# Optimization experiments

Measured on AMD Instinct MI355X. Metric: run time of the kernel, lower is better.

The kernel has to match this reference:

```python
import jax, jax.numpy as jnp
import numpy as np

DIM = 512
NUM_HEADS = 8
NUM_BLOCKS = 16
# NOTE: original code computes head_dim from FULL dim (before the reduce layer),
# so scale = (dim // num_heads) ** -0.5 = 64 ** -0.5, even though the actual
# per-head dim after reduce is 32. We preserve this quirk faithfully.
SCALE = (DIM // NUM_HEADS) ** -0.5


def setup_inputs() -> dict:
    key = jax.random.key(0)
    ks = jax.random.split(key, 5)
    B, N = 4, 4096
    C = DIM // 2
    x = jax.random.normal(ks[0], (B, N, DIM), dtype=jnp.float32)
    reduce_w = jax.random.normal(ks[1], (DIM, C), dtype=jnp.float32) * (DIM ** -0.5)
    qkv_w = jax.random.normal(ks[2], (C, 3 * C), dtype=jnp.float32) * (C ** -0.5)
    proj_w = jax.random.normal(ks[3], (C, DIM), dtype=jnp.float32) * (C ** -0.5)
    proj_b = jnp.zeros((DIM,), dtype=jnp.float32)
    return {"x": x, "reduce_w": reduce_w, "qkv_w": qkv_w,
            "proj_w": proj_w, "proj_b": proj_b}


def reference(x, reduce_w, qkv_w, proj_w, proj_b):
    B, N, _ = x.shape
    xr = x @ reduce_w                      # [B, N, C]  (C = dim/2)
    C = xr.shape[-1]
    H = NUM_HEADS
    d = C // H
    qkv = (xr @ qkv_w).reshape(B, N, 3, H, d).transpose(2, 0, 3, 1, 4)  # [3,B,H,N,d]
    q, k, v = qkv[0], qkv[1], qkv[2]
    bs = N // NUM_BLOCKS                   # block (chunk) size
    # block-diagonal local attention: reshape seq into independent blocks
    qb = q.reshape(B, H, NUM_BLOCKS, bs, d)
    kb = k.reshape(B, H, NUM_BLOCKS, bs, d)
    vb = v.reshape(B, H, NUM_BLOCKS, bs, d)
    attn = jnp.einsum('bhnqd,bhnkd->bhnqk', qb, kb) * SCALE
    attn = jax.nn.softmax(attn, axis=-1)
    ob = jnp.einsum('bhnqk,bhnkd->bhnqd', attn, vb)   # [B,H,Nb,bs,d]
    # torch: per-block transpose(1,2) then cat on dim=1 -> [B, N, H, d]
    o = ob.transpose(0, 2, 3, 1, 4).reshape(B, N, C)
    return o @ proj_w + proj_b
```

## Files before the change

### kernel.cpp

```cpp
#include <hip/hip_runtime.h>
#include <hip/hip_fp16.h>

typedef _Float16 half_t;
typedef _Float16 f16x8 __attribute__((ext_vector_type(8)));
typedef __fp16 fp16x2 __attribute__((ext_vector_type(2)));
typedef float f32x4 __attribute__((ext_vector_type(4)));

#define MFMA_F16(a, b, c) __builtin_amdgcn_mfma_f32_16x16x32_f16((a), (b), (c), 0, 0, 0)

static __device__ inline unsigned pkrtz(float a, float b) {
    union { fp16x2 h; unsigned u; } c;
    c.h = __builtin_amdgcn_cvt_pkrtz(a, b);
    return c.u;
}

__global__ __launch_bounds__(256) void prep(
    const float* __restrict__ qw, const float* __restrict__ rw,
    const float* __restrict__ pw, half_t* __restrict__ pw_t,
    half_t* __restrict__ Wt) {
    __shared__ __align__(16) char smem[24576];
    const int bid = blockIdx.x, tid = threadIdx.x;

    if (bid < 48) {
        char* As = smem;
        char* Bs = smem + 8192;
        const int M0 = (bid % 12) * 64, N0 = (bid / 12) * 128;
        const int lane = tid & 63, w = tid >> 6;
        const int l15 = lane & 15, l4 = lane >> 4;
        const int wrow = (w >> 1) * 32, wcol = (w & 1) * 64;
        const int pa = (l15 & 7) << 4;

        f32x4 acc[2][4];
#pragma unroll
        for (int i = 0; i < 2; ++i)
#pragma unroll
            for (int j = 0; j < 4; ++j) acc[i][j] = (f32x4){0.f, 0.f, 0.f, 0.f};

        for (int kc = 0; kc < 4; ++kc) {
            int c0 = kc * 64;
            __syncthreads();
#pragma unroll
            for (int i = 0; i < 2; ++i) {
                int j = tid + i * 256;
                int row = j >> 3, e8 = (j & 7) * 8;
                float s = (M0 + row) < 256 ? 0.18033688f : 1.f;
                f16x8 v;
#pragma unroll
                for (int e = 0; e < 8; ++e)
                    v[e] = (half_t)(qw[(size_t)(c0 + e8 + e) * 768 + M0 + row] * s);
                *(f16x8*)(As + row * 128 + ((e8 * 2) ^ ((row & 7) << 4))) = v;
            }
#pragma unroll
            for (int i = 0; i < 4; ++i) {
                int j = tid + i * 256;
                int row = j >> 3, e8 = (j & 7) * 8;
                const float* p = rw + (size_t)(N0 + row) * 256 + c0 + e8;
                float4 u0 = *(const float4*)p;
                float4 u1 = *(const float4*)(p + 4);
                f16x8 v;
                v[0] = (half_t)u0.x; v[1] = (half_t)u0.y;
                v[2] = (half_t)u0.z; v[3] = (half_t)u0.w;
                v[4] = (half_t)u1.x; v[5] = (half_t)u1.y;
                v[6] = (half_t)u1.z; v[7] = (half_t)u1.w;
                *(f16x8*)(Bs + row * 128 + ((e8 * 2) ^ ((row & 7) << 4))) = v;
            }
            __syncthreads();
#pragma unroll
            for (int ki = 0; ki < 2; ++ki) {
                f16x8 af[2], bf[4];
#pragma unroll
                for (int mi = 0; mi < 2; ++mi) {
                    int row = wrow + mi * 16 + l15;
                    af[mi] = *(const f16x8*)(As + row * 128 + (((ki * 4 + l4) << 4) ^ pa));
                }
#pragma unroll
                for (int nj = 0; nj < 4; ++nj) {
                    int row = wcol + nj * 16 + l15;
                    bf[nj] = *(const f16x8*)(Bs + row * 128 + (((ki * 4 + l4) << 4) ^ pa));
                }
#pragma unroll
                for (int mi = 0; mi < 2; ++mi)
#pragma unroll
                    for (int nj = 0; nj < 4; ++nj)
                        acc[mi][nj] = MFMA_F16(af[mi], bf[nj], acc[mi][nj]);
            }
        }
#pragma unroll
        for (int mi = 0; mi < 2; ++mi)
#pragma unroll
            for (int nj = 0; nj < 4; ++nj)
#pragma unroll
                for (int reg = 0; reg < 4; ++reg) {
                    int grow = M0 + wrow + mi * 16 + l4 * 4 + reg;
                    int gcol = N0 + wcol + nj * 16 + l15;
                    Wt[(size_t)grow * 512 + gcol] = (half_t)acc[mi][nj][reg];
                }
        return;
    }

    half_t* tile = (half_t*)smem;
    int t = bid - 48;
    int R0 = (t >> 3) * 64, C0 = (t & 7) * 64;
#pragma unroll
    for (int e = 0; e < 16; ++e) {
        int idx = tid + e * 256;
        int r = idx >> 6, c = idx & 63;
        tile[r * 72 + c] = (half_t)pw[(size_t)(R0 + r) * 512 + C0 + c];
    }
    __syncthreads();
#pragma unroll
    for (int e = 0; e < 16; ++e) {
        int idx = tid + e * 256;
        int c = idx >> 6, r = idx & 63;
        pw_t[(size_t)(C0 + c) * 256 + R0 + r] = tile[r * 72 + c];
    }
}

template <int EPI, bool AFP32, int NB, int K>
__global__ __launch_bounds__(512) void gemm_f16(
    const void* __restrict__ Aop, const half_t* __restrict__ Bt,
    void* __restrict__ Dst, const float* __restrict__ bias) {
    constexpr int nkt = K >> 6;
    constexpr int NAC = 2;
    constexpr int NBC = NB / 64;
    constexpr int NJ = NB / 64;
    __shared__ __align__(16) char smem[16384 + NB * 128];
    char* As = smem;
    char* Bs = smem + 16384;

    const int tid = threadIdx.x;
    const int lane = tid & 63, w = tid >> 6;
    const int l15 = lane & 15, l4 = lane >> 4;
    const int wrow = (w >> 2) * 64;
    const int wcol = (w & 3) * (NB / 4);
    const int bm0 = blockIdx.x * 128;
    const int bn0 = blockIdx.y * NB;
    const int pa = (l15 & 7) << 4;

    f32x4 acc[4][NJ];
#pragma unroll
    for (int i = 0; i < 4; ++i)
#pragma unroll
        for (int j = 0; j < NJ; ++j) acc[i][j] = (f32x4){0.f, 0.f, 0.f, 0.f};

    f16x8 aReg[NAC], bReg[NBC];

    auto load_tile = [&](int kt) {
#pragma unroll
        for (int i = 0; i < NAC; ++i) {
            int c = tid + i * 512;
            int row = c >> 3, k0 = (c & 7) * 8;
            int gk = kt * 64 + k0;
            if (AFP32) {
                const float* Af = (const float*)Aop + (size_t)(bm0 + row) * K + gk;
                float4 u0 = *(const float4*)Af;
                float4 u1 = *(const float4*)(Af + 4);
                f16x8 v;
                v[0] = (half_t)u0.x; v[1] = (half_t)u0.y;
                v[2] = (half_t)u0.z; v[3] = (half_t)u0.w;
                v[4] = (half_t)u1.x; v[5] = (half_t)u1.y;
                v[6] = (half_t)u1.z; v[7] = (half_t)u1.w;
                aReg[i] = v;
            } else {
                aReg[i] = *(const f16x8*)((const half_t*)Aop + (size_t)(bm0 + row) * K + gk);
            }
        }
#pragma unroll
        for (int i = 0; i < NBC; ++i) {
            int c = tid + i * 512;
            int row = c >> 3, k0 = (c & 7) * 8;
            bReg[i] = *(const f16x8*)(Bt + (size_t)(bn0 + row) * K + kt * 64 + k0);
        }
    };

    load_tile(0);
    for (int kt = 0; kt < nkt; ++kt) {
        __syncthreads();
#pragma unroll
        for (int i = 0; i < NAC; ++i) {
            int c = tid + i * 512;
            int row = c >> 3, k0 = (c & 7) * 8;
            *(f16x8*)(As + row * 128 + ((k0 * 2) ^ ((row & 7) << 4))) = aReg[i];
        }
#pragma unroll
        for (int i = 0; i < NBC; ++i) {
            int c = tid + i * 512;
            int row = c >> 3, k0 = (c & 7) * 8;
            *(f16x8*)(Bs + row * 128 + ((k0 * 2) ^ ((row & 7) << 4))) = bReg[i];
        }
        __syncthreads();
        if (kt + 1 < nkt) load_tile(kt + 1);
#pragma unroll
        for (int ki = 0; ki < 2; ++ki) {
            f16x8 af[4], bf[NJ];
#pragma unroll
            for (int mi = 0; mi < 4; ++mi) {
                int row = wrow + mi * 16 + l15;
                af[mi] = *(const f16x8*)(As + row * 128 + (((ki * 4 + l4) << 4) ^ pa));
            }
#pragma unroll
            for (int nj = 0; nj < NJ; ++nj) {
                int row = wcol + nj * 16 + l15;
                bf[nj] = *(const f16x8*)(Bs + row * 128 + (((ki * 4 + l4) << 4) ^ pa));
            }
#pragma unroll
            for (int mi = 0; mi < 4; ++mi)
#pragma unroll
                for (int nj = 0; nj < NJ; ++nj)
                    acc[mi][nj] = MFMA_F16(af[mi], bf[nj], acc[mi][nj]);
        }
    }

#pragma unroll
    for (int mi = 0; mi < 4; ++mi) {
#pragma unroll
        for (int nj = 0; nj < NJ; ++nj) {
#pragma unroll
            for (int reg = 0; reg < 4; ++reg) {
                int grow = bm0 + wrow + mi * 16 + l4 * 4 + reg;
                int gcol = bn0 + wcol + nj * 16 + l15;
                float val = acc[mi][nj][reg];
                if (EPI == 1) {
                    int t = gcol >> 8, h = (gcol >> 5) & 7, dd = gcol & 31;
                    int b = grow >> 12, n = grow & 4095;
                    int blk = n >> 8, r = n & 255;
                    size_t idx = (size_t)t * 4194304 +
                                 (size_t)((((b << 3) + h) << 4) + blk) * 8192 +
                                 (size_t)r * 32 + dd;
                    ((half_t*)Dst)[idx] = (half_t)val;
                } else {
                    ((float*)Dst)[(size_t)grow * 512 + gcol] = val + bias[gcol];
                }
            }
        }
    }
}

__global__ __launch_bounds__(512, 4) void attn_f16(const half_t* __restrict__ qkv_ws,
                                                   half_t* __restrict__ o_ws) {
    __shared__ __align__(16) half_t VT[32 * 264];

    const int blkid = blockIdx.x;
    const int b = blkid >> 7, h = (blkid >> 4) & 7, blk = blkid & 15;
    const half_t* Q  = qkv_ws + (size_t)blkid * 8192;
    const half_t* Kp = qkv_ws + 4194304 + (size_t)blkid * 8192;
    const half_t* V  = qkv_ws + 8388608 + (size_t)blkid * 8192;

    const int tid = threadIdx.x, lane = tid & 63, w = tid >> 6;
    const int l15 = lane & 15, l4 = lane >> 4;
    const int qb = w * 32;

#pragma unroll
    for (int i = 0; i < 2; ++i) {
        int c = tid + i * 512;
        int key = c >> 2, k8 = (c & 3) * 8;
        f16x8 v = *(const f16x8*)(V + key * 32 + k8);
#pragma unroll
        for (int e = 0; e < 8; ++e) VT[(k8 + e) * 264 + key] = v[e];
    }

    f16x8 aq[2];
    aq[0] = *(const f16x8*)(Q + (qb + l15) * 32 + l4 * 8);
    aq[1] = *(const f16x8*)(Q + (qb + 16 + l15) * 32 + l4 * 8);

    __syncthreads();

    float s_run[2] = {0.f, 0.f};
    f32x4 acc_o[2][2];
#pragma unroll
    for (int qg = 0; qg < 2; ++qg)
#pragma unroll
        for (int fo = 0; fo < 2; ++fo) acc_o[qg][fo] = (f32x4){0.f, 0.f, 0.f, 0.f};
    const f32x4 zero4 = (f32x4){0.f, 0.f, 0.f, 0.f};

    for (int kt = 0; kt < 4; ++kt) {
        f16x8 ka[4];
#pragma unroll
        for (int t = 0; t < 4; ++t)
            ka[t] = *(const f16x8*)(Kp + (kt * 64 + t * 16 + l15) * 32 + l4 * 8);
        f16x8 bv[2][2];
#pragma unroll
        for (int c = 0; c < 2; ++c)
#pragma unroll
            for (int fo = 0; fo < 2; ++fo)
                bv[c][fo] = *(const f16x8*)&VT[(fo * 16 + l15) * 264 + kt * 64 + c * 32 + l4 * 8];

        f32x4 st[2][4];
        __builtin_amdgcn_s_setprio(1);
#pragma unroll
        for (int qg = 0; qg < 2; ++qg)
#pragma unroll
            for (int t = 0; t < 4; ++t) st[qg][t] = MFMA_F16(ka[t], aq[qg], zero4);
        __builtin_amdgcn_s_setprio(0);

#pragma unroll
        for (int qg = 0; qg < 2; ++qg) {
            float p[4][4];
            float ps = 0.f;
#pragma unroll
            for (int t = 0; t < 4; ++t)
#pragma unroll
                for (int r = 0; r < 4; ++r) {
                    float e = exp2f(st[qg][t][r]);
                    p[t][r] = e;
                    ps += e;
                }
            ps += __shfl_xor(ps, 16);
            ps += __shfl_xor(ps, 32);
            s_run[qg] += ps;

#pragma unroll
            for (int c = 0; c < 2; ++c) {
                unsigned pk0[2], pk1[2];
#pragma unroll
                for (int rp = 0; rp < 2; ++rp) {
                    pk0[rp] = pkrtz(p[2 * c][2 * rp], p[2 * c][2 * rp + 1]);
                    pk1[rp] = pkrtz(p[2 * c + 1][2 * rp], p[2 * c + 1][2 * rp + 1]);
                }
                union { unsigned u[4]; f16x8 v; } au;
#pragma unroll
                for (int j = 0; j < 4; ++j) {
                    int src = l15 + ((((l4 & 1) << 1) + (j >> 1)) << 4);
                    unsigned g0 = (unsigned)__shfl((int)pk0[j & 1], src);
                    unsigned g1 = (unsigned)__shfl((int)pk1[j & 1], src);
                    au.u[j] = (l4 < 2) ? g0 : g1;
                }
                __builtin_amdgcn_s_setprio(1);
#pragma unroll
                for (int fo = 0; fo < 2; ++fo)
                    acc_o[qg][fo] = MFMA_F16(au.v, bv[c][fo], acc_o[qg][fo]);
                __builtin_amdgcn_s_setprio(0);
            }
        }
    }

#pragma unroll
    for (int qg = 0; qg < 2; ++qg) {
        float inv = 1.f / s_run[qg];
        float sinv[4];
#pragma unroll
        for (int r = 0; r < 4; ++r) sinv[r] = __shfl(inv, (l4 << 2) | r);
#pragma unroll
        for (int fo = 0; fo < 2; ++fo)
#pragma unroll
            for (int r = 0; r < 4; ++r) {
                int grow = b * 4096 + blk * 256 + qb + qg * 16 + l4 * 4 + r;
                o_ws[(size_t)grow * 256 + h * 32 + fo * 16 + l15] =
                    (half_t)(acc_o[qg][fo][r] * sinv[r]);
            }
    }
}

extern "C" void kernel_launch(void* const* d_in, const int* in_sizes, int n_in,
                              void* d_out, int out_size, void* d_ws, size_t ws_size,
                              hipStream_t stream) {
    const float* x        = (const float*)d_in[0];
    const float* reduce_w = (const float*)d_in[1];
    const float* qkv_w    = (const float*)d_in[2];
    const float* proj_w   = (const float*)d_in[3];
    const float* proj_b   = (const float*)d_in[4];
    char* ws = (char*)d_ws;

    half_t* qkv_ws = (half_t*)ws;
    half_t* o_buf  = (half_t*)(ws + 25165824);
    half_t* pw_t   = (half_t*)(ws + 33554432);
    half_t* Wt     = (half_t*)(ws + 33816576);

    prep<<<80, 256, 0, stream>>>(qkv_w, reduce_w, proj_w, pw_t, Wt);
    gemm_f16<1, true, 192, 512><<<dim3(128, 4), 512, 0, stream>>>(x, Wt, qkv_ws, nullptr);
    attn_f16<<<512, 512, 0, stream>>>(qkv_ws, o_buf);
    gemm_f16<2, false, 256, 256><<<dim3(128, 2), 512, 0, stream>>>(o_buf, pw_t, d_out, proj_b);
}
```

Baseline: 61.71 us.

## Rewrite QKV GEMM with 32x32 MFMA and 256-row tiles

Replaces the templated GEMM with a dedicated QKV kernel that uses 32x32x16 MFMA instructions, a 256x192 block tile with a 4x2 wave layout, and swizzled global-to-LDS chunk mapping. This halves the grid to 256 blocks, so each block reuses the weight tile across more rows and issues fewer MFMA instructions per FLOP. The projection GEMM is specialised into its own non-templated kernel with unchanged logic. The trade-offs are larger LDS and register use per block and fewer blocks to spread across the CUs.

After: 62.96 us. +2.0%, slower.

```diff
diff --git a/kernel.cpp b/kernel.cpp
--- a/kernel.cpp
+++ b/kernel.cpp
@@ -5,8 +5,10 @@
 typedef _Float16 f16x8 __attribute__((ext_vector_type(8)));
 typedef __fp16 fp16x2 __attribute__((ext_vector_type(2)));
 typedef float f32x4 __attribute__((ext_vector_type(4)));
+typedef float f32x16 __attribute__((ext_vector_type(16)));
 
 #define MFMA_F16(a, b, c) __builtin_amdgcn_mfma_f32_16x16x32_f16((a), (b), (c), 0, 0, 0)
+#define MFMA32_F16(a, b, c) __builtin_amdgcn_mfma_f32_32x32x16_f16((a), (b), (c), 0, 0, 0)
 
 static __device__ inline unsigned pkrtz(float a, float b) {
     union { fp16x2 h; unsigned u; } c;
@@ -116,124 +118,195 @@
     }
 }
 
-template <int EPI, bool AFP32, int NB, int K>
-__global__ __launch_bounds__(512) void gemm_f16(
-    const void* __restrict__ Aop, const half_t* __restrict__ Bt,
-    void* __restrict__ Dst, const float* __restrict__ bias) {
-    constexpr int nkt = K >> 6;
-    constexpr int NAC = 2;
-    constexpr int NBC = NB / 64;
-    constexpr int NJ = NB / 64;
-    __shared__ __align__(16) char smem[16384 + NB * 128];
+__global__ __launch_bounds__(512) void gemm_qkv(
+    const float* __restrict__ X, const half_t* __restrict__ Bt,
+    half_t* __restrict__ Dst) {
+    __shared__ __align__(16) char smem[32768 + 24576];
+    char* As = smem;
+    char* Bs = smem + 32768;
+
+    const int tid = threadIdx.x;
+    const int lane = tid & 63, wv = tid >> 6;
+    const int l31 = lane & 31, kh = lane >> 5;
+    const int wrow = (wv >> 1) * 64, wcol = (wv & 1) * 96;
+    const int bm0 = blockIdx.x * 256;
+    const int bn0 = blockIdx.y * 192;
+
+    f32x16 acc[2][3];
+#pragma unroll
+    for (int i = 0; i < 2; ++i)
+#pragma unroll
+        for (int j = 0; j < 3; ++j) acc[i][j] = (f32x16)(0.f);
+
+    f16x8 aReg[4], bReg[3];
+
+    auto load_tile = [&](int kt) {
+#pragma unroll
+        for (int i = 0; i < 4; ++i) {
+            int J = tid + i * 512;
+            int row = J >> 3, c = (J & 7) ^ (row & 7);
+            const float* p = X + (size_t)(bm0 + row) * 512 + kt * 64 + c * 8;
+            float4 u0 = *(const float4*)p;
+            float4 u1 = *(const float4*)(p + 4);
+            f16x8 v;
+            v[0] = (half_t)u0.x; v[1] = (half_t)u0.y;
+            v[2] = (half_t)u0.z; v[3] = (half_t)u0.w;
+            v[4] = (half_t)u1.x; v[5] = (half_t)u1.y;
+            v[6] = (half_t)u1.z; v[7] = (half_t)u1.w;
+            aReg[i] = v;
+        }
+#pragma unroll
+        for (int i = 0; i < 3; ++i) {
+            int J = tid + i * 512;
+            int row = J >> 3, c = (J & 7) ^ (row & 7);
+            bReg[i] = *(const f16x8*)(Bt + (size_t)(bn0 + row) * 512 + kt * 64 + c * 8);
+        }
+    };
+
+    load_tile(0);
+    for (int kt = 0; kt < 8; ++kt) {
+        __syncthreads();
+#pragma unroll
+        for (int i = 0; i < 4; ++i) {
+            int J = tid + i * 512;
+            *(f16x8*)(As + J * 16) = aReg[i];
+        }
+#pragma unroll
+        for (int i = 0; i < 3; ++i) {
+            int J = tid + i * 512;
+            *(f16x8*)(Bs + J * 16) = bReg[i];
+        }
+        __syncthreads();
+        if (kt + 1 < 8) load_tile(kt + 1);
+#pragma unroll
+        for (int ks = 0; ks < 4; ++ks) {
+            int chunk = ks * 2 + kh;
+            f16x8 af[2], bf[3];
+#pragma unroll
+            for (int mt = 0; mt < 2; ++mt) {
+                int row = wrow + mt * 32 + l31;
+                af[mt] = *(const f16x8*)(As + row * 128 + ((chunk ^ (row & 7)) << 4));
+            }
+#pragma unroll
+            for (int nt = 0; nt < 3; ++nt) {
+                int row = wcol + nt * 32 + l31;
+                bf[nt] = *(const f16x8*)(Bs + row * 128 + ((chunk ^ (row & 7)) << 4));
+            }
+#pragma unroll
+            for (int mt = 0; mt < 2; ++mt)
+#pragma unroll
+                for (int nt = 0; nt < 3; ++nt)
+                    acc[mt][nt] = MFMA32_F16(af[mt], bf[nt], acc[mt][nt]);
+        }
+    }
+
+#pragma unroll
+    for (int mt = 0; mt < 2; ++mt) {
+#pragma unroll
+        for (int nt = 0; nt < 3; ++nt) {
+#pragma unroll
+            for (int reg = 0; reg < 16; ++reg) {
+                int grow = bm0 + wrow + mt * 32 + (reg & 3) + 8 * (reg >> 2) + 4 * kh;
+                int gcol = bn0 + wcol + nt * 32 + l31;
+                float val = acc[mt][nt][reg];
+                int t = gcol >> 8, h = (gcol >> 5) & 7, dd = gcol & 31;
+                int b = grow >> 12, n = grow & 4095;
+                int blk = n >> 8, r = n & 255;
+                size_t idx = (size_t)t * 4194304 +
+                             (size_t)((((b << 3) + h) << 4) + blk) * 8192 +
+                             (size_t)r * 32 + dd;
+                Dst[idx] = (half_t)val;
+            }
+        }
+    }
+}
+
+__global__ __launch_bounds__(512) void gemm_proj(
+    const half_t* __restrict__ A, const half_t* __restrict__ Bt,
+    float* __restrict__ Dst, const float* __restrict__ bias) {
+    __shared__ __align__(16) char smem[16384 + 32768];
     char* As = smem;
     char* Bs = smem + 16384;
 
     const int tid = threadIdx.x;
     const int lane = tid & 63, w = tid >> 6;
     const int l15 = lane & 15, l4 = lane >> 4;
-    const int wrow = (w >> 2) * 64;
-    const int wcol = (w & 3) * (NB / 4);
+    const int wrow = (w >> 2) * 64, wcol = (w & 3) * 64;
     const int bm0 = blockIdx.x * 128;
-    const int bn0 = blockIdx.y * NB;
+    const int bn0 = blockIdx.y * 256;
     const int pa = (l15 & 7) << 4;
 
-    f32x4 acc[4][NJ];
+    f32x4 acc[4][4];
 #pragma unroll
     for (int i = 0; i < 4; ++i)
 #pragma unroll
-        for (int j = 0; j < NJ; ++j) acc[i][j] = (f32x4){0.f, 0.f, 0.f, 0.f};
-
-    f16x8 aReg[NAC], bReg[NBC];
+        for (int j = 0; j < 4; ++j) acc[i][j] = (f32x4){0.f, 0.f, 0.f, 0.f};
+
+    f16x8 aReg[2], bReg[4];
 
     auto load_tile = [&](int kt) {
 #pragma unroll
-        for (int i = 0; i < NAC; ++i) {
+        for (int i = 0; i < 2; ++i) {
             int c = tid + i * 512;
             int row = c >> 3, k0 = (c & 7) * 8;
-            int gk = kt * 64 + k0;
-            if (AFP32) {
-                const float* Af = (const float*)Aop + (size_t)(bm0 + row) * K + gk;
-                float4 u0 = *(const float4*)Af;
-                float4 u1 = *(const float4*)(Af + 4);
-                f16x8 v;
-                v[0] = (half_t)u0.x; v[1] = (half_t)u0.y;
-                v[2] = (half_t)u0.z; v[3] = (half_t)u0.w;
-                v[4] = (half_t)u1.x; v[5] = (half_t)u1.y;
-                v[6] = (half_t)u1.z; v[7] = (half_t)u1.w;
-                aReg[i] = v;
-            } else {
-                aReg[i] = *(const f16x8*)((const half_t*)Aop + (size_t)(bm0 + row) * K + gk);
-            }
-        }
-#pragma unroll
-        for (int i = 0; i < NBC; ++i) {
+            aReg[i] = *(const f16x8*)(A + (size_t)(bm0 + row) * 256 + kt * 64 + k0);
+        }
+#pragma unroll
+        for (int i = 0; i < 4; ++i) {
             int c = tid + i * 512;
             int row = c >> 3, k0 = (c & 7) * 8;
-            bReg[i] = *(const f16x8*)(Bt + (size_t)(bn0 + row) * K + kt * 64 + k0);
+            bReg[i] = *(const f16x8*)(Bt + (size_t)(bn0 + row) * 256 + kt * 64 + k0);
         }
     };
 
     load_tile(0);
-    for (int kt = 0; kt < nkt; ++kt) {
+    for (int kt = 0; kt < 4; ++kt) {
         __syncthreads();
 #pragma unroll
-        for (int i = 0; i < NAC; ++i) {
+        for (int i = 0; i < 2; ++i) {
             int c = tid + i * 512;
             int row = c >> 3, k0 = (c & 7) * 8;
             *(f16x8*)(As + row * 128 + ((k0 * 2) ^ ((row & 7) << 4))) = aReg[i];
         }
 #pragma unroll
-        for (int i = 0; i < NBC; ++i) {
+        for (int i = 0; i < 4; ++i) {
             int c = tid + i * 512;
             int row = c >> 3, k0 = (c & 7) * 8;
             *(f16x8*)(Bs + row * 128 + ((k0 * 2) ^ ((row & 7) << 4))) = bReg[i];
         }
         __syncthreads();
-        if (kt + 1 < nkt) load_tile(kt + 1);
+        if (kt + 1 < 4) load_tile(kt + 1);
 #pragma unroll
         for (int ki = 0; ki < 2; ++ki) {
-            f16x8 af[4], bf[NJ];
+            f16x8 af[4], bf[4];
 #pragma unroll
             for (int mi = 0; mi < 4; ++mi) {
                 int row = wrow + mi * 16 + l15;
                 af[mi] = *(const f16x8*)(As + row * 128 + (((ki * 4 + l4) << 4) ^ pa));
             }
 #pragma unroll
-            for (int nj = 0; nj < NJ; ++nj) {
+            for (int nj = 0; nj < 4; ++nj) {
                 int row = wcol + nj * 16 + l15;
                 bf[nj] = *(const f16x8*)(Bs + row * 128 + (((ki * 4 + l4) << 4) ^ pa));
             }
 #pragma unroll
             for (int mi = 0; mi < 4; ++mi)
 #pragma unroll
-                for (int nj = 0; nj < NJ; ++nj)
+                for (int nj = 0; nj < 4; ++nj)
                     acc[mi][nj] = MFMA_F16(af[mi], bf[nj], acc[mi][nj]);
         }
     }
 
 #pragma unroll
-    for (int mi = 0; mi < 4; ++mi) {
-#pragma unroll
-        for (int nj = 0; nj < NJ; ++nj) {
+    for (int mi = 0; mi < 4; ++mi)
+#pragma unroll
+        for (int nj = 0; nj < 4; ++nj)
 #pragma unroll
             for (int reg = 0; reg < 4; ++reg) {
                 int grow = bm0 + wrow + mi * 16 + l4 * 4 + reg;
                 int gcol = bn0 + wcol + nj * 16 + l15;
-                float val = acc[mi][nj][reg];
-                if (EPI == 1) {
-                    int t = gcol >> 8, h = (gcol >> 5) & 7, dd = gcol & 31;
-                    int b = grow >> 12, n = grow & 4095;
-                    int blk = n >> 8, r = n & 255;
-                    size_t idx = (size_t)t * 4194304 +
-                                 (size_t)((((b << 3) + h) << 4) + blk) * 8192 +
-                                 (size_t)r * 32 + dd;
-                    ((half_t*)Dst)[idx] = (half_t)val;
-                } else {
-                    ((float*)Dst)[(size_t)grow * 512 + gcol] = val + bias[gcol];
-                }
-            }
-        }
-    }
+                Dst[(size_t)grow * 512 + gcol] = acc[mi][nj][reg] + bias[gcol];
+            }
 }
 
 __global__ __launch_bounds__(512, 4) void attn_f16(const half_t* __restrict__ qkv_ws,
@@ -367,7 +440,7 @@
     half_t* Wt     = (half_t*)(ws + 33816576);
 
     prep<<<80, 256, 0, stream>>>(qkv_w, reduce_w, proj_w, pw_t, Wt);
-    gemm_f16<1, true, 192, 512><<<dim3(128, 4), 512, 0, stream>>>(x, Wt, qkv_ws, nullptr);
+    gemm_qkv<<<dim3(64, 4), 512, 0, stream>>>(x, Wt, qkv_ws);
     attn_f16<<<512, 512, 0, stream>>>(qkv_ws, o_buf);
-    gemm_f16<2, false, 256, 256><<<dim3(128, 2), 512, 0, stream>>>(o_buf, pw_t, d_out, proj_b);
-}
+    gemm_proj<<<dim3(128, 2), 512, 0, stream>>>(o_buf, pw_t, (float*)d_out, proj_b);
+}
```
